# Kernel tuning notes

Hardware: AMD Instinct MI355X
Metric: run time of the kernel (lower is better)

The kernel has to match this reference:

```python
import jax, jax.numpy as jnp
import numpy as np

B, N, D, R = 2, 256, 128, 32

def _sh_l1(r):
    # e3nn-style component-normalized l=1 spherical harmonics of unit vectors
    return jnp.sqrt(3.0) * r

def _sh_l2(r):
    x, y, z = r[..., 0], r[..., 1], r[..., 2]
    c = jnp.sqrt(15.0)
    return jnp.stack([
        c * x * y,
        c * y * z,
        0.5 * jnp.sqrt(5.0) * (3.0 * z * z - 1.0),  # x^2+y^2+z^2 = 1
        c * x * z,
        0.5 * c * (x * x - y * y),
    ], axis=-1)

def _radial(rbf, w1, b1, w2, b2):
    h = rbf @ w1 + b1
    return (h * jax.nn.sigmoid(h)) @ w2 + b2  # Linear -> SiLU -> Linear

def _layernorm(x, g, b, eps=1e-5):
    m = jnp.mean(x, axis=-1, keepdims=True)
    v = jnp.var(x, axis=-1, keepdims=True)
    return (x - m) * jax.lax.rsqrt(v + eps) * g + b

def setup_inputs() -> dict:
    key = jax.random.key(0)
    ks = iter(jax.random.split(key, 40))
    def nrm(shape, s=1.0):
        return jax.random.normal(next(ks), shape, dtype=jnp.float32) * s
    r_hat = nrm((B, N, N, 3))
    r_hat = r_hat / (jnp.linalg.norm(r_hat, axis=-1, keepdims=True) + 1e-9)
    inp = {
        'node_s': nrm((B, N, D)),
        'node_v': nrm((B, N, 3, D)),
        'node_t': nrm((B, N, 5, D)),
        'rbf': jax.random.uniform(next(ks), (B, N, N, R), dtype=jnp.float32),
        'r_hat': r_hat,
        'mask': jnp.ones((B, N, N), dtype=jnp.float32),
    }
    s1, s2 = 1.0 / np.sqrt(R), 1.0 / np.sqrt(D)
    for p in ('r0', 'r1', 'r2', 'r110'):
        inp[p + '_w1'] = nrm((R, D), s1)
        inp[p + '_b1'] = jnp.zeros((D,), jnp.float32)
        inp[p + '_w2'] = nrm((D, D), s2)
        inp[p + '_b2'] = jnp.zeros((D,), jnp.float32)
    inp['src_w'] = nrm((D, D), s2)
    inp['ln_g'] = jnp.ones((D,), jnp.float32)
    inp['ln_b'] = jnp.zeros((D,), jnp.float32)
    inp['out_w'] = nrm((D, D), s2)
    inp['out_b'] = jnp.zeros((D,), jnp.float32)
    inp['v_scale'] = jnp.ones((D,), jnp.float32)
    inp['t_scale'] = jnp.ones((D,), jnp.float32)
    return inp

def reference(node_s, node_v, node_t, rbf, r_hat, mask,
              r0_w1, r0_b1, r0_w2, r0_b2,
              r1_w1, r1_b1, r1_w2, r1_b2,
              r2_w1, r2_b1, r2_w2, r2_b2,
              r110_w1, r110_b1, r110_w2, r110_b2,
              src_w, ln_g, ln_b, out_w, out_b, v_scale, t_scale):
    h = node_s @ src_w                               # (B,N,D)
    h_j = h[:, None, :, :] * mask[..., None]         # (B,N,N,D): h_j[b,i,j]=h[b,j]*mask[b,i,j]
    Y1 = _sh_l1(r_hat)                               # (B,N,N,3)
    Y2 = _sh_l2(r_hat)                               # (B,N,N,5)

    msg_s = jnp.sum(h_j * _radial(rbf, r0_w1, r0_b1, r0_w2, r0_b2), axis=2)  # (B,N,D)
    delta_v = jnp.einsum('bijd,bijc->bicd',
                         h_j * _radial(rbf, r1_w1, r1_b1, r1_w2, r1_b2), Y1) * v_scale
    delta_t = jnp.einsum('bijd,bijc->bicd',
                         h_j * _radial(rbf, r2_w1, r2_b1, r2_w2, r2_b2), Y2) * t_scale

    # v_j[b,i,j] = node_v[b,i] (per the torch unsqueeze(2).expand)
    dot_vY1 = jnp.einsum('bicd,bijc->bijd', node_v, Y1)                      # (B,N,N,D)
    msg_s_from_v = jnp.sum(dot_vY1 * _radial(rbf, r110_w1, r110_b1, r110_w2, r110_b2)
                           * mask[..., None], axis=2)                        # (B,N,D)

    delta_s = _layernorm(msg_s + msg_s_from_v, ln_g, ln_b) @ out_w + out_b
    return (delta_s, delta_v, delta_t)
```

## Files before the change

### kernel.cpp

```cpp
#include <hip/hip_runtime.h>

#define Bb 2
#define Nn 256
#define Dd 128
#define Rr 32

typedef unsigned short u16;
typedef unsigned int   u32;
typedef __attribute__((ext_vector_type(8))) short bf16x8;
typedef __attribute__((ext_vector_type(4))) short bf16x4;
typedef __attribute__((ext_vector_type(4))) float f32x4;
typedef __attribute__((ext_vector_type(2))) u32   u32x2;

__device__ __forceinline__ short f2bfs(float f){
  u32 u = __float_as_uint(f);
  u += 0x7FFFu + ((u >> 16) & 1u);
  return (short)(u >> 16);
}
__device__ __forceinline__ u16 f2bf(float f){
  u32 u = __float_as_uint(f);
  u += 0x7FFFu + ((u >> 16) & 1u);
  return (u16)(u >> 16);
}

__global__ __launch_bounds__(128) void hproj_kernel(
    const float* __restrict__ node_s, const float* __restrict__ src_w,
    float* __restrict__ h_out){
  __shared__ float s_row[Dd];
  const int bi = blockIdx.x, d = threadIdx.x;
  s_row[d] = node_s[(size_t)bi*Dd + d];
  __syncthreads();
  float acc = 0.f;
  #pragma unroll 8
  for (int k=0;k<Dd;k++) acc += s_row[k]*src_w[k*Dd + d];
  h_out[(size_t)bi*Dd + d] = acc;
}

__global__ __launch_bounds__(256,2) void se3_mfma3(
    const float* __restrict__ node_v,
    const float* __restrict__ rbf,
    const float* __restrict__ r_hat,
    const float* __restrict__ maskp,
    const float* __restrict__ r0w1, const float* __restrict__ r0b1,
    const float* __restrict__ r0w2, const float* __restrict__ r0b2,
    const float* __restrict__ r1w1, const float* __restrict__ r1b1,
    const float* __restrict__ r1w2, const float* __restrict__ r1b2,
    const float* __restrict__ r2w1, const float* __restrict__ r2b1,
    const float* __restrict__ r2w2, const float* __restrict__ r2b2,
    const float* __restrict__ r3w1, const float* __restrict__ r3b1,
    const float* __restrict__ r3w2, const float* __restrict__ r3b2,
    const float* __restrict__ ln_g, const float* __restrict__ ln_b,
    const float* __restrict__ out_w, const float* __restrict__ out_b,
    const float* __restrict__ v_scale, const float* __restrict__ t_scale,
    const float* __restrict__ h_ws,
    float* __restrict__ out_s, float* __restrict__ out_v, float* __restrict__ out_t)
{
  __shared__ u16   s_rbf[Nn*36];
  __shared__ u16   s_hid[64*136];
  __shared__ u16   s_YT[10*264];
  __shared__ u16   s_Y1r[3*264];
  __shared__ u16   s_G[4*32*72];
  __shared__ float s_msg[Dd];
  __shared__ float s_xn[Dd];
  __shared__ float s_part[2*Dd];
  __shared__ float s_mv[2];

  const int tid  = threadIdx.x;
  const int bi   = blockIdx.x;
  const int b    = bi >> 8;
  const int lane = tid & 63;
  const int w    = tid >> 6;
  const int q    = lane >> 4;
  const int cc   = lane & 15;
  const int dbase= w*32;

  {
    int j = tid;
    size_t pidx = (size_t)bi*Nn + j;
    float mk = maskp[pidx];
    float x = r_hat[pidx*3+0];
    float y = r_hat[pidx*3+1];
    float z = r_hat[pidx*3+2];
    const float SQ3=1.7320508075688772f;
    const float C15=3.8729833462074170f;
    const float C5H=1.1180339887498949f;
    float y1a=SQ3*x, y1b=SQ3*y, y1c=SQ3*z;
    s_YT[0*264+j]=f2bf(mk);
    s_YT[1*264+j]=f2bf(y1a*mk);
    s_YT[2*264+j]=f2bf(y1b*mk);
    s_YT[3*264+j]=f2bf(y1c*mk);
    s_YT[4*264+j]=f2bf(C15*x*y*mk);
    s_YT[5*264+j]=f2bf(C15*y*z*mk);
    s_YT[6*264+j]=f2bf(C5H*(3.f*z*z-1.f)*mk);
    s_YT[7*264+j]=f2bf(C15*x*z*mk);
    s_YT[8*264+j]=f2bf(0.5f*C15*(x*x-y*y)*mk);
    s_YT[9*264+j]=f2bf(mk);
    s_Y1r[0*264+j]=f2bf(y1a);
    s_Y1r[1*264+j]=f2bf(y1b);
    s_Y1r[2*264+j]=f2bf(y1c);
  }

  const float* rbf_blk = rbf + (size_t)bi*Nn*Rr;
  const float* hb      = h_ws + (size_t)b*Nn*Dd;

  for (int idx=tid; idx<Nn*Rr; idx+=256){
    int j = idx >> 5, r = idx & 31;
    s_rbf[j*36 + r] = f2bf(rbf_blk[idx]);
  }

  bf16x8 vBf[2];
  {
    const float* nv = node_v + (size_t)bi*3*Dd;
    #pragma unroll
    for (int nt=0;nt<2;nt++){
      int dd = dbase+nt*16+cc;
      bf16x8 t = {0,0,0,0,0,0,0,0};
      if (q==0){
        t[0]=f2bfs(nv[0*Dd+dd]);
        t[1]=f2bfs(nv[1*Dd+dd]);
        t[2]=f2bfs(nv[2*Dd+dd]);
      }
      vBf[nt]=t;
    }
  }

  const f32x4 zf = {0.f,0.f,0.f,0.f};
  f32x4 accred[2] = {zf, zf};

  #pragma unroll 1
  for (int p=0;p<4;p++){
    const float* W1p = (p==0)?r0w1:(p==1)?r1w1:(p==2)?r2w1:r3w1;
    const float* B1p = (p==0)?r0b1:(p==1)?r1b1:(p==2)?r2b1:r3b1;
    const float* W2p = (p==0)?r0w2:(p==1)?r1w2:(p==2)?r2w2:r3w2;
    const float* B2p = (p==0)?r0b2:(p==1)?r1b2:(p==2)?r2b2:r3b2;
    const int lo = (p==0)?0:(p==1)?1:(p==2)?4:9;
    const int hi = (p==0)?0:(p==1)?3:(p==2)?8:9;
    const u32 gmask = (cc>=lo && cc<=hi) ? 0xFFFFFFFFu : 0u;
    const u16* ytrow = &s_YT[(cc<10?cc:9)*264];

    bf16x8 w1f[2];
    bf16x8 w2f[2][4];
    float  b1v[2], b2v[2];
    #pragma unroll
    for (int nt=0;nt<2;nt++){
      int dd = dbase+nt*16+cc;
      b1v[nt]=B1p[dd];
      b2v[nt]=B2p[dd];
      #pragma unroll
      for (int jj=0;jj<8;jj++)
        w1f[nt][jj] = f2bfs(W1p[(q*8+jj)*Dd + dd]);
      #pragma unroll
      for (int ks=0;ks<4;ks++){
        #pragma unroll
        for (int jj=0;jj<8;jj++)
          w2f[nt][ks][jj] = f2bfs(W2p[(ks*32+q*8+jj)*Dd + dd]);
      }
    }

    #pragma unroll 1
    for (int ch=0; ch<4; ch++){
      __syncthreads();
      #pragma unroll
      for (int m=0;m<4;m++){
        const u16* ap = &s_rbf[(ch*64 + m*16 + cc)*36 + q*8];
        bf16x4 lo4 = *(const bf16x4*)ap;
        bf16x4 hi4 = *(const bf16x4*)(ap+4);
        bf16x8 raf = {lo4[0],lo4[1],lo4[2],lo4[3],hi4[0],hi4[1],hi4[2],hi4[3]};
        #pragma unroll
        for (int nt=0;nt<2;nt++){
          f32x4 hc = __builtin_amdgcn_mfma_f32_16x16x32_bf16(raf, w1f[nt], zf, 0,0,0);
          #pragma unroll
          for (int r=0;r<4;r++){
            float x  = hc[r] + b1v[nt];
            float e  = __expf(-x);
            float s  = x*__builtin_amdgcn_rcpf(1.f+e);
            s_hid[(m*16+q*4+r)*136 + dbase + nt*16 + cc] = f2bf(s);
          }
        }
      }
      __syncthreads();
      #pragma unroll
      for (int m=0;m<4;m++){
        bf16x8 af[4];
        #pragma unroll
        for (int ks=0;ks<4;ks++)
          af[ks] = *(const bf16x8*)&s_hid[(m*16+cc)*136 + ks*32 + q*8];

        f32x4 dotC[2];
        if (p==3){
          bf16x8 aY = {0,0,0,0,0,0,0,0};
          if (q==0){
            int j = ch*64 + m*16 + cc;
            aY[0]=(short)s_Y1r[0*264+j];
            aY[1]=(short)s_Y1r[1*264+j];
            aY[2]=(short)s_Y1r[2*264+j];
          }
          #pragma unroll
          for (int nt=0;nt<2;nt++)
            dotC[nt] = __builtin_amdgcn_mfma_f32_16x16x32_bf16(aY, vBf[nt], zf, 0,0,0);
        }

        #pragma unroll
        for (int nt=0;nt<2;nt++){
          f32x4 c2 = zf;
          #pragma unroll
          for (int ks=0;ks<4;ks++)
            c2 = __builtin_amdgcn_mfma_f32_16x16x32_bf16(af[ks], w2f[nt][ks], c2, 0,0,0);
          int dd = dbase+nt*16+cc;
          u16 g4[4];
          if (p<3){
            const float* hp = hb + (size_t)(ch*64 + m*16 + q*4)*Dd + dd;
            #pragma unroll
            for (int r=0;r<4;r++)
              g4[r] = f2bf((c2[r]+b2v[nt]) * hp[(size_t)r*Dd]);
          } else {
            #pragma unroll
            for (int r=0;r<4;r++)
              g4[r] = f2bf((c2[r]+b2v[nt]) * dotC[nt][r]);
          }
          u32x2 pk = { (u32)g4[0] | ((u32)g4[1]<<16),
                       (u32)g4[2] | ((u32)g4[3]<<16) };
          *(u32x2*)&s_G[(w*32 + nt*16 + cc)*72 + m*16 + q*4] = pk;
        }
      }
      #pragma unroll
      for (int ks2=0;ks2<2;ks2++){
        bf16x8 aR = *(const bf16x8*)(ytrow + ch*64 + ks2*32 + q*8);
        u32* arp = (u32*)&aR;
        arp[0]&=gmask; arp[1]&=gmask; arp[2]&=gmask; arp[3]&=gmask;
        #pragma unroll
        for (int nt=0;nt<2;nt++){
          bf16x8 bG = *(const bf16x8*)&s_G[(w*32 + nt*16 + cc)*72 + ks2*32 + q*8];
          accred[nt] = __builtin_amdgcn_mfma_f32_16x16x32_bf16(aR, bG, accred[nt], 0,0,0);
        }
      }
    }
  }

  #pragma unroll
  for (int nt=0;nt<2;nt++){
    int d = dbase + nt*16 + cc;
    #pragma unroll
    for (int r=0;r<4;r++){
      int rw = q*4 + r;
      float val = accred[nt][r];
      if (rw==0)      s_msg[d] = val;
      else if (rw<=3) out_v[(size_t)bi*3*Dd + (size_t)(rw-1)*Dd + d] = val*v_scale[d];
      else if (rw<=8) out_t[(size_t)bi*5*Dd + (size_t)(rw-4)*Dd + d] = val*t_scale[d];
      else if (rw==9) s_xn[d] = val;
    }
  }
  __syncthreads();

  if (tid < 64){
    float a0=s_msg[tid]+s_xn[tid], a1=s_msg[tid+64]+s_xn[tid+64];
    float s1=a0+a1, s2=a0*a0+a1*a1;
    #pragma unroll
    for (int off=1;off<64;off<<=1){
      s1 += __shfl_xor(s1,off);
      s2 += __shfl_xor(s2,off);
    }
    if (tid==0){
      float m   = s1*(1.f/Dd);
      float var = fmaxf(s2*(1.f/Dd) - m*m, 0.f);
      s_mv[0]=m;
      s_mv[1]=rsqrtf(var+1e-5f);
    }
  }
  __syncthreads();
  if (tid < Dd){
    float msg = s_msg[tid]+s_xn[tid];
    s_xn[tid] = (msg - s_mv[0])*s_mv[1]*ln_g[tid] + ln_b[tid];
  }
  __syncthreads();

  {
    int dp = tid & 127, seg = tid >> 7;
    float pa = 0.f;
    #pragma unroll 8
    for (int k=seg*64;k<seg*64+64;k++)
      pa += s_xn[k]*out_w[k*Dd+dp];
    s_part[seg*Dd+dp]=pa;
  }
  __syncthreads();
  if (tid < Dd)
    out_s[(size_t)bi*Dd+tid] = s_part[tid]+s_part[Dd+tid]+out_b[tid];
}

extern "C" void kernel_launch(void* const* d_in, const int* in_sizes, int n_in,
                              void* d_out, int out_size, void* d_ws, size_t ws_size,
                              hipStream_t stream) {
  const float* node_s = (const float*)d_in[0];
  const float* node_v = (const float*)d_in[1];
  const float* rbf    = (const float*)d_in[3];
  const float* r_hat  = (const float*)d_in[4];
  const float* maskp  = (const float*)d_in[5];
  const float* r0w1=(const float*)d_in[6],  *r0b1=(const float*)d_in[7];
  const float* r0w2=(const float*)d_in[8],  *r0b2=(const float*)d_in[9];
  const float* r1w1=(const float*)d_in[10], *r1b1=(const float*)d_in[11];
  const float* r1w2=(const float*)d_in[12], *r1b2=(const float*)d_in[13];
  const float* r2w1=(const float*)d_in[14], *r2b1=(const float*)d_in[15];
  const float* r2w2=(const float*)d_in[16], *r2b2=(const float*)d_in[17];
  const float* r3w1=(const float*)d_in[18], *r3b1=(const float*)d_in[19];
  const float* r3w2=(const float*)d_in[20], *r3b2=(const float*)d_in[21];
  const float* src_w  =(const float*)d_in[22];
  const float* ln_g   =(const float*)d_in[23];
  const float* ln_b   =(const float*)d_in[24];
  const float* out_w  =(const float*)d_in[25];
  const float* out_b  =(const float*)d_in[26];
  const float* v_scale=(const float*)d_in[27];
  const float* t_scale=(const float*)d_in[28];

  float* h_ws = (float*)d_ws;
  float* out_s = (float*)d_out;
  float* out_v = out_s + (size_t)Bb*Nn*Dd;
  float* out_t = out_v + (size_t)Bb*Nn*3*Dd;

  hproj_kernel<<<dim3(Bb*Nn), dim3(Dd), 0, stream>>>(node_s, src_w, h_ws);
  se3_mfma3<<<dim3(Bb*Nn), dim3(256), 0, stream>>>(
      node_v, rbf, r_hat, maskp,
      r0w1,r0b1,r0w2,r0b2, r1w1,r1b1,r1w2,r1b2,
      r2w1,r2b1,r2w2,r2b2, r3w1,r3b1,r3w2,r3b2,
      ln_g, ln_b, out_w, out_b, v_scale, t_scale,
      h_ws, out_s, out_v, out_t);
}
```

Baseline: 196.0 us.

## Pre-transpose radial weights to bf16 and split row tiles across 8 waves

```diff
diff --git a/kernel.cpp b/kernel.cpp
--- a/kernel.cpp
+++ b/kernel.cpp
@@ -12,6 +12,9 @@
 typedef __attribute__((ext_vector_type(4))) float f32x4;
 typedef __attribute__((ext_vector_type(2))) u32   u32x2;
 
+__device__ u16 g_w1t[4*Dd*Rr];
+__device__ u16 g_w2t[4*Dd*Dd];
+
 __device__ __forceinline__ short f2bfs(float f){
   u32 u = __float_as_uint(f);
   u += 0x7FFFu + ((u >> 16) & 1u);
@@ -23,32 +26,53 @@
   return (u16)(u >> 16);
 }
 
-__global__ __launch_bounds__(128) void hproj_kernel(
+__global__ __launch_bounds__(128) void prep_kernel(
     const float* __restrict__ node_s, const float* __restrict__ src_w,
-    float* __restrict__ h_out){
-  __shared__ float s_row[Dd];
-  const int bi = blockIdx.x, d = threadIdx.x;
-  s_row[d] = node_s[(size_t)bi*Dd + d];
-  __syncthreads();
-  float acc = 0.f;
-  #pragma unroll 8
-  for (int k=0;k<Dd;k++) acc += s_row[k]*src_w[k*Dd + d];
-  h_out[(size_t)bi*Dd + d] = acc;
-}
-
-__global__ __launch_bounds__(256,2) void se3_mfma3(
+    const float* __restrict__ r0w1, const float* __restrict__ r1w1,
+    const float* __restrict__ r2w1, const float* __restrict__ r3w1,
+    const float* __restrict__ r0w2, const float* __restrict__ r1w2,
+    const float* __restrict__ r2w2, const float* __restrict__ r3w2,
+    float* __restrict__ h_out)
+{
+  const int bx = blockIdx.x;
+  const int t  = threadIdx.x;
+  if (bx < Bb*Nn){
+    __shared__ float s_row[Dd];
+    s_row[t] = node_s[(size_t)bx*Dd + t];
+    __syncthreads();
+    float acc = 0.f;
+    #pragma unroll 8
+    for (int k=0;k<Dd;k++) acc += s_row[k]*src_w[k*Dd + t];
+    h_out[(size_t)bx*Dd + t] = acc;
+  } else {
+    const int kb = bx - Bb*Nn;
+    const int p  = kb >> 3, sl = kb & 7;
+    const float* W1 = (p==0)?r0w1:(p==1)?r1w1:(p==2)?r2w1:r3w1;
+    const float* W2 = (p==0)?r0w2:(p==1)?r1w2:(p==2)?r2w2:r3w2;
+    u16* W1T = g_w1t + p*Dd*Rr;
+    u16* W2T = g_w2t + p*Dd*Dd;
+    #pragma unroll
+    for (int it=0; it<4; it++){
+      int idx = sl*512 + it*128 + t;
+      W1T[idx] = f2bf(W1[(idx & 31)*Dd + (idx >> 5)]);
+    }
+    #pragma unroll
+    for (int it=0; it<16; it++){
+      int idx = sl*2048 + it*128 + t;
+      W2T[idx] = f2bf(W2[(idx & 127)*Dd + (idx >> 7)]);
+    }
+  }
+}
+
+__global__ __launch_bounds__(512,4) void se3_mfma8(
     const float* __restrict__ node_v,
     const float* __restrict__ rbf,
     const float* __restrict__ r_hat,
     const float* __restrict__ maskp,
-    const float* __restrict__ r0w1, const float* __restrict__ r0b1,
-    const float* __restrict__ r0w2, const float* __restrict__ r0b2,
-    const float* __restrict__ r1w1, const float* __restrict__ r1b1,
-    const float* __restrict__ r1w2, const float* __restrict__ r1b2,
-    const float* __restrict__ r2w1, const float* __restrict__ r2b1,
-    const float* __restrict__ r2w2, const float* __restrict__ r2b2,
-    const float* __restrict__ r3w1, const float* __restrict__ r3b1,
-    const float* __restrict__ r3w2, const float* __restrict__ r3b2,
+    const float* __restrict__ r0b1, const float* __restrict__ r0b2,
+    const float* __restrict__ r1b1, const float* __restrict__ r1b2,
+    const float* __restrict__ r2b1, const float* __restrict__ r2b2,
+    const float* __restrict__ r3b1, const float* __restrict__ r3b2,
     const float* __restrict__ ln_g, const float* __restrict__ ln_b,
     const float* __restrict__ out_w, const float* __restrict__ out_b,
     const float* __restrict__ v_scale, const float* __restrict__ t_scale,
@@ -59,10 +83,11 @@
   __shared__ u16   s_hid[64*136];
   __shared__ u16   s_YT[10*264];
   __shared__ u16   s_Y1r[3*264];
-  __shared__ u16   s_G[4*32*72];
+  __shared__ u16   s_G[128*72];
+  __shared__ float s_red[16*130];
   __shared__ float s_msg[Dd];
   __shared__ float s_xn[Dd];
-  __shared__ float s_part[2*Dd];
+  __shared__ float s_part[4*Dd];
   __shared__ float s_mv[2];
 
   const int tid  = threadIdx.x;
@@ -72,9 +97,11 @@
   const int w    = tid >> 6;
   const int q    = lane >> 4;
   const int cc   = lane & 15;
-  const int dbase= w*32;
-
-  {
+  const int mpair= w & 1;
+  const int dgrp = w >> 1;
+  const int dbase= dgrp*32;
+
+  if (tid < Nn){
     int j = tid;
     size_t pidx = (size_t)bi*Nn + j;
     float mk = maskp[pidx];
@@ -103,7 +130,7 @@
   const float* rbf_blk = rbf + (size_t)bi*Nn*Rr;
   const float* hb      = h_ws + (size_t)b*Nn*Dd;
 
-  for (int idx=tid; idx<Nn*Rr; idx+=256){
+  for (int idx=tid; idx<Nn*Rr; idx+=512){
     int j = idx >> 5, r = idx & 31;
     s_rbf[j*36 + r] = f2bf(rbf_blk[idx]);
   }
@@ -129,10 +156,10 @@
 
   #pragma unroll 1
   for (int p=0;p<4;p++){
-    const float* W1p = (p==0)?r0w1:(p==1)?r1w1:(p==2)?r2w1:r3w1;
     const float* B1p = (p==0)?r0b1:(p==1)?r1b1:(p==2)?r2b1:r3b1;
-    const float* W2p = (p==0)?r0w2:(p==1)?r1w2:(p==2)?r2w2:r3w2;
     const float* B2p = (p==0)?r0b2:(p==1)?r1b2:(p==2)?r2b2:r3b2;
+    const u16* W1T = g_w1t + p*Dd*Rr;
+    const u16* W2T = g_w2t + p*Dd*Dd;
     const int lo = (p==0)?0:(p==1)?1:(p==2)?4:9;
     const int hi = (p==0)?0:(p==1)?3:(p==2)?8:9;
     const u32 gmask = (cc>=lo && cc<=hi) ? 0xFFFFFFFFu : 0u;
@@ -146,22 +173,18 @@
       int dd = dbase+nt*16+cc;
       b1v[nt]=B1p[dd];
       b2v[nt]=B2p[dd];
+      w1f[nt] = *(const bf16x8*)&W1T[dd*Rr + q*8];
       #pragma unroll
-      for (int jj=0;jj<8;jj++)
-        w1f[nt][jj] = f2bfs(W1p[(q*8+jj)*Dd + dd]);
-      #pragma unroll
-      for (int ks=0;ks<4;ks++){
-        #pragma unroll
-        for (int jj=0;jj<8;jj++)
-          w2f[nt][ks][jj] = f2bfs(W2p[(ks*32+q*8+jj)*Dd + dd]);
-      }
+      for (int ks=0;ks<4;ks++)
+        w2f[nt][ks] = *(const bf16x8*)&W2T[dd*Dd + ks*32 + q*8];
     }
 
     #pragma unroll 1
     for (int ch=0; ch<4; ch++){
       __syncthreads();
       #pragma unroll
-      for (int m=0;m<4;m++){
+      for (int mm=0;mm<2;mm++){
+        const int m = mpair*2 + mm;
         const u16* ap = &s_rbf[(ch*64 + m*16 + cc)*36 + q*8];
         bf16x4 lo4 = *(const bf16x4*)ap;
         bf16x4 hi4 = *(const bf16x4*)(ap+4);
@@ -179,8 +202,9 @@
         }
       }
       __syncthreads();
-      #pragma unroll
-      for (int m=0;m<4;m++){
+      #pragma unroll 1
+      for (int mm=0;mm<2;mm++){
+        const int m = mpair*2 + mm;
         bf16x8 af[4];
         #pragma unroll
         for (int ks=0;ks<4;ks++)
@@ -206,7 +230,7 @@
           #pragma unroll
           for (int ks=0;ks<4;ks++)
             c2 = __builtin_amdgcn_mfma_f32_16x16x32_bf16(af[ks], w2f[nt][ks], c2, 0,0,0);
-          int dd = dbase+nt*16+cc;
+          const int dd = dbase+nt*16+cc;
           u16 g4[4];
           if (p<3){
             const float* hp = hb + (size_t)(ch*64 + m*16 + q*4)*Dd + dd;
@@ -220,34 +244,45 @@
           }
           u32x2 pk = { (u32)g4[0] | ((u32)g4[1]<<16),
                        (u32)g4[2] | ((u32)g4[3]<<16) };
-          *(u32x2*)&s_G[(w*32 + nt*16 + cc)*72 + m*16 + q*4] = pk;
+          *(u32x2*)&s_G[(size_t)(dd)*72 + m*16 + q*4] = pk;
         }
       }
-      #pragma unroll
-      for (int ks2=0;ks2<2;ks2++){
-        bf16x8 aR = *(const bf16x8*)(ytrow + ch*64 + ks2*32 + q*8);
+      {
+        bf16x8 aR = *(const bf16x8*)(ytrow + ch*64 + mpair*32 + q*8);
         u32* arp = (u32*)&aR;
         arp[0]&=gmask; arp[1]&=gmask; arp[2]&=gmask; arp[3]&=gmask;
         #pragma unroll
         for (int nt=0;nt<2;nt++){
-          bf16x8 bG = *(const bf16x8*)&s_G[(w*32 + nt*16 + cc)*72 + ks2*32 + q*8];
+          bf16x8 bG = *(const bf16x8*)&s_G[(size_t)(dbase + nt*16 + cc)*72 + mpair*32 + q*8];
           accred[nt] = __builtin_amdgcn_mfma_f32_16x16x32_bf16(aR, bG, accred[nt], 0,0,0);
         }
       }
     }
   }
 
-  #pragma unroll
-  for (int nt=0;nt<2;nt++){
-    int d = dbase + nt*16 + cc;
-    #pragma unroll
-    for (int r=0;r<4;r++){
-      int rw = q*4 + r;
-      float val = accred[nt][r];
-      if (rw==0)      s_msg[d] = val;
-      else if (rw<=3) out_v[(size_t)bi*3*Dd + (size_t)(rw-1)*Dd + d] = val*v_scale[d];
-      else if (rw<=8) out_t[(size_t)bi*5*Dd + (size_t)(rw-4)*Dd + d] = val*t_scale[d];
-      else if (rw==9) s_xn[d] = val;
+  if (mpair){
+    #pragma unroll
+    for (int nt=0;nt<2;nt++){
+      const int d = dbase + nt*16 + cc;
+      #pragma unroll
+      for (int r=0;r<4;r++)
+        s_red[(q*4+r)*130 + d] = accred[nt][r];
+    }
+  }
+  __syncthreads();
+  if (!mpair){
+    #pragma unroll
+    for (int nt=0;nt<2;nt++){
+      const int d = dbase + nt*16 + cc;
+      #pragma unroll
+      for (int r=0;r<4;r++){
+        const int rw = q*4 + r;
+        float val = accred[nt][r] + s_red[rw*130 + d];
+        if (rw==0)      s_msg[d] = val;
+        else if (rw<=3) out_v[(size_t)bi*3*Dd + (size_t)(rw-1)*Dd + d] = val*v_scale[d];
+        else if (rw<=8) out_t[(size_t)bi*5*Dd + (size_t)(rw-4)*Dd + d] = val*t_scale[d];
+        else if (rw==9) s_xn[d] = val;
+      }
     }
   }
   __syncthreads();
@@ -278,13 +313,13 @@
     int dp = tid & 127, seg = tid >> 7;
     float pa = 0.f;
     #pragma unroll 8
-    for (int k=seg*64;k<seg*64+64;k++)
+    for (int k=seg*32;k<seg*32+32;k++)
       pa += s_xn[k]*out_w[k*Dd+dp];
     s_part[seg*Dd+dp]=pa;
   }
   __syncthreads();
   if (tid < Dd)
-    out_s[(size_t)bi*Dd+tid] = s_part[tid]+s_part[Dd+tid]+out_b[tid];
+    out_s[(size_t)bi*Dd+tid] = s_part[tid]+s_part[Dd+tid]+s_part[2*Dd+tid]+s_part[3*Dd+tid]+out_b[tid];
 }
 
 extern "C" void kernel_launch(void* const* d_in, const int* in_sizes, int n_in,
@@ -316,11 +351,13 @@
   float* out_v = out_s + (size_t)Bb*Nn*Dd;
   float* out_t = out_v + (size_t)Bb*Nn*3*Dd;
 
-  hproj_kernel<<<dim3(Bb*Nn), dim3(Dd), 0, stream>>>(node_s, src_w, h_ws);
-  se3_mfma3<<<dim3(Bb*Nn), dim3(256), 0, stream>>>(
+  prep_kernel<<<dim3(Bb*Nn + 32), dim3(128), 0, stream>>>(
+      node_s, src_w,
+      r0w1, r1w1, r2w1, r3w1, r0w2, r1w2, r2w2, r3w2,
+      h_ws);
+  se3_mfma8<<<dim3(Bb*Nn), dim3(512), 0, stream>>>(
       node_v, rbf, r_hat, maskp,
-      r0w1,r0b1,r0w2,r0b2, r1w1,r1b1,r1w2,r1b2,
-      r2w1,r2b1,r2w2,r2b2, r3w1,r3b1,r3w2,r3b2,
+      r0b1,r0b2, r1b1,r1b2, r2b1,r2b2, r3b1,r3b2,
       ln_g, ln_b, out_w, out_b, v_scale, t_scale,
       h_ws, out_s, out_v, out_t);
 }
```

Result: no change. 198.3 us (+1.2%).
